# Performance work log

Hardware: AMD Instinct MI355X
Metric: run time of the kernel (lower is better)

## Reference

```python
import jax, jax.numpy as jnp
import numpy as np

N, C, H, W = 32, 256, 64, 64
STRIDE = 4  # slices of refs' H dim per block, as in the torch mem_save path
EPS = 1e-12  # F.normalize clamp_min eps


def setup_inputs() -> dict:
    key = jax.random.key(0)
    k1, k2 = jax.random.split(key)
    refs = jax.random.normal(k1, (N, C, H, W), dtype=jnp.float32)
    img = jax.random.normal(k2, (C, H, W), dtype=jnp.float32)
    return {"refs": refs, "img": img}


def _l2_normalize(x, axis):
    # matches torch.nn.functional.normalize(p=2): x / max(||x||, eps)
    n = jnp.sqrt(jnp.sum(x * x, axis=axis, keepdims=True))
    return x / jnp.maximum(n, EPS)


def reference(refs, img):
    # refs: (N, C, H, W), img: (C, H, W)
    refs_n = _l2_normalize(refs, axis=1)
    img_n = _l2_normalize(img, axis=0)

    img_flat = img_n.reshape(C, H * W).T  # (HW, C) query vectors

    # group reference feature vectors by blocks of STRIDE rows of refs' H dim:
    # (N,C,H,W) -> (H, N, W, C) -> (H//STRIDE, STRIDE*N*W, C)
    blocks = refs_n.transpose(2, 0, 3, 1).reshape(H // STRIDE, STRIDE * N * W, C)

    def step(running_max, block):
        # (HW, C) x (blocksize, C)^T -> (HW, blocksize) cosine sims
        sim = jnp.einsum('xc,yc->xy', img_flat, block)
        return jnp.maximum(running_max, sim.max(axis=1)), None

    init = jnp.full((H * W,), -jnp.inf, dtype=img_flat.dtype)
    best, _ = jax.lax.scan(step, init, blocks)
    return best.reshape(H, W)
```

## Files before the change

### kernel.cpp

```cpp
#include <hip/hip_runtime.h>

#define CN 256
#define HN 64
#define WN 64
#define NNW 32
#define HW (HN*WN)
#define NREF (NNW*HW)
#define KD 256

#define BMT 128
#define BNT 64
#define NCHV 16
#define NTILES (NREF/NCHV/BNT)

using bf16x8 = __attribute__((ext_vector_type(8))) short;
using f32x4  = __attribute__((ext_vector_type(4))) float;

__device__ inline unsigned short f2bf(float x) {
  unsigned int u = __float_as_uint(x);
  return (unsigned short)((u + 0x7fffu + ((u >> 16) & 1u)) >> 16);
}

__device__ inline void atomicMaxFloat(float* addr, float val) {
  if (val >= 0.f) atomicMax(reinterpret_cast<int*>(addr), __float_as_int(val));
  else            atomicMin(reinterpret_cast<unsigned int*>(addr), __float_as_uint(val));
}

__device__ inline void gload_lds16(const void* g, void* l) {
  __builtin_amdgcn_global_load_lds(
      (const __attribute__((address_space(1))) void*)g,
      (__attribute__((address_space(3))) void*)l, 16, 0, 0);
}

__global__ __launch_bounds__(256)
void norm_kernel(const float* __restrict__ refs, const float* __restrict__ img,
                 unsigned short* __restrict__ Rb, unsigned short* __restrict__ Qb,
                 float* __restrict__ out) {
  __shared__ float tile[CN][WN + 1];
  __shared__ float ssq[4][WN];
  __shared__ float scl[WN];
  const int bid = blockIdx.x;
  const int t = threadIdx.x;
  const float* src; unsigned short* dst; int nh;
  if (bid < NNW * HN) { src = refs; dst = Rb; nh = bid; }
  else {
    src = img; dst = Qb; nh = bid - NNW * HN;
    if (t < 64) out[(size_t)nh * 64 + t] = -INFINITY;
  }
  const float* base = src + (size_t)(nh >> 6) * (CN * (size_t)HW) + (size_t)(nh & 63) * WN;

  const int c16 = t >> 4, w4 = (t & 15) * 4;
#pragma unroll
  for (int j = 0; j < 16; ++j) {
    int c = j * 16 + c16;
    float4 v = *(const float4*)&base[(size_t)c * HW + w4];
    tile[c][w4 + 0] = v.x; tile[c][w4 + 1] = v.y;
    tile[c][w4 + 2] = v.z; tile[c][w4 + 3] = v.w;
  }
  __syncthreads();
  {
    int w = t & 63, vv = t >> 6;
    float s = 0.f;
#pragma unroll 8
    for (int cc = 0; cc < 64; ++cc) { float x = tile[vv * 64 + cc][w]; s += x * x; }
    ssq[vv][w] = s;
  }
  __syncthreads();
  if (t < 64)
    scl[t] = 1.f / fmaxf(sqrtf(ssq[0][t] + ssq[1][t] + ssq[2][t] + ssq[3][t]), 1e-12f);
  __syncthreads();
  const int w = t >> 2, cq = t & 3;
  unsigned short* orow = dst + ((size_t)nh * WN + w) * KD;
  const float sc = scl[w];
#pragma unroll
  for (int j = 0; j < 8; ++j) {
    int c0 = (j * 4 + cq) * 8;
    bf16x8 o;
#pragma unroll
    for (int k = 0; k < 8; ++k) o[k] = (short)f2bf(tile[c0 + k][w] * sc);
    *(bf16x8*)&orow[c0] = o;
  }
}

#define BARR() __builtin_amdgcn_s_barrier()
#define SCHED0() __builtin_amdgcn_sched_barrier(0)
#define GATE(N) asm volatile("s_waitcnt vmcnt(" #N ")" ::: "memory")
#define LGKM0() asm volatile("s_waitcnt lgkmcnt(0)" ::: "memory")

#define STGB(P, BT) do { \
  _Pragma("unroll") \
  for (int q = 0; q < 8; ++q) \
    gload_lds16(rsb + (BT) * 16384 + q * 2048, &lds[P][wid * 4096 + q * 512]); \
} while (0)

#define STRIP(P, NI) do { \
  bf16x8 bb[8]; \
  _Pragma("unroll") \
  for (int kf = 0; kf < 8; ++kf) \
    bb[kf] = *(const bf16x8*)&lds[P][(kf >> 1) * 4096 + ((NI) * 16 + l15) * 64 \
        + ((((kf & 1) * 4 + (lane >> 4)) ^ l7) * 8)]; \
  f32x4 acc0, acc1; \
  __builtin_amdgcn_s_setprio(1); \
  _Pragma("unroll") \
  for (int kf = 0; kf < 8; ++kf) { \
    acc0 = __builtin_amdgcn_mfma_f32_16x16x32_bf16(a[0][kf], bb[kf], kf ? acc0 : ZZ, 0, 0, 0); \
    acc1 = __builtin_amdgcn_mfma_f32_16x16x32_bf16(a[1][kf], bb[kf], kf ? acc1 : ZZ, 0, 0, 0); \
  } \
  __builtin_amdgcn_s_setprio(0); \
  _Pragma("unroll") \
  for (int ee = 0; ee < 4; ++ee) { \
    run0[ee] = fmaxf(run0[ee], acc0[ee]); \
    run1[ee] = fmaxf(run1[ee], acc1[ee]); \
  } \
} while (0)

#define STRIPS(P) do { STRIP(P, 0); STRIP(P, 1); STRIP(P, 2); STRIP(P, 3); } while (0)

__global__ __launch_bounds__(256, 2)
void simmax_kernel(const unsigned short* __restrict__ Q,
                   const unsigned short* __restrict__ R,
                   float* __restrict__ out) {
  __shared__ unsigned short lds[2][16384];

  const int t = threadIdx.x;
  const int lane = t & 63;
  const int wid = t >> 6;
  const int l15 = lane & 15;
  const int l7  = lane & 7;

  const int wg  = (blockIdx.x & 7) * 64 + (blockIdx.x >> 3);
  const int nch = wg >> 5;
  const int bm  = wg & 31;

  const int srow = lane >> 3;
  const int schunk = (lane & 7) ^ srow;
  const unsigned short* rsb = R + ((size_t)nch * 8192 + srow) * KD + wid * 64 + schunk * 8;

  const f32x4 ZZ = {0.f, 0.f, 0.f, 0.f};
  f32x4 run0, run1;
#pragma unroll
  for (int ee = 0; ee < 4; ++ee) { run0[ee] = -1e30f; run1[ee] = -1e30f; }

#pragma unroll
  for (int b = 0; b < 2; ++b) {
    const unsigned short* qsb = Q + (size_t)(bm * BMT + b * 64 + srow) * KD
                                  + wid * 64 + schunk * 8;
#pragma unroll
    for (int q = 0; q < 8; ++q)
      gload_lds16(qsb + q * 2048, &lds[b][wid * 4096 + q * 512]);
  }
  GATE(0); BARR(); SCHED0();

  bf16x8 a[2][8];
#pragma unroll
  for (int mi = 0; mi < 2; ++mi) {
    const int row = wid * 32 + mi * 16 + l15;
    const int r63 = row & 63;
#pragma unroll
    for (int kf = 0; kf < 8; ++kf)
      a[mi][kf] = *(const bf16x8*)&lds[wid >> 1][(kf >> 1) * 4096 + r63 * 64
          + ((((kf & 1) * 4 + (lane >> 4)) ^ l7) * 8)];
  }
  LGKM0(); BARR();

  STGB(0, 0);
  for (int bt = 0; bt < NTILES - 1; ++bt) {
    STGB((bt + 1) & 1, bt + 1);
    GATE(8); BARR(); SCHED0();
    STRIPS(bt & 1);
    BARR();
  }
  GATE(0); BARR(); SCHED0();
  STRIPS((NTILES - 1) & 1);

#pragma unroll
  for (int mi = 0; mi < 2; ++mi)
#pragma unroll
    for (int ee = 0; ee < 4; ++ee) {
      float v = mi ? run1[ee] : run0[ee];
      v = fmaxf(v, __shfl_xor(v, 1));
      v = fmaxf(v, __shfl_xor(v, 2));
      v = fmaxf(v, __shfl_xor(v, 4));
      v = fmaxf(v, __shfl_xor(v, 8));
      if (l15 == 0)
        atomicMaxFloat(&out[bm * BMT + wid * 32 + mi * 16 + (lane >> 4) * 4 + ee], v);
    }
}

extern "C" void kernel_launch(void* const* d_in, const int* in_sizes, int n_in,
                              void* d_out, int out_size, void* d_ws, size_t ws_size,
                              hipStream_t stream) {
  const float* refs = (const float*)d_in[0];
  const float* img  = (const float*)d_in[1];
  float* out = (float*)d_out;

  unsigned short* Rb = (unsigned short*)d_ws;
  unsigned short* Qb = Rb + (size_t)NREF * KD;

  hipLaunchKernelGGL(norm_kernel, dim3(NNW * HN + HN), dim3(256), 0, stream,
                     refs, img, Rb, Qb, out);
  hipLaunchKernelGGL(simmax_kernel, dim3(NCHV * (HW / BMT)), dim3(256), 0, stream,
                     Qb, Rb, out);
}
```

Baseline: 251.7 us.

## Double the query tile per workgroup to 256 rows and split refs into 32 chunks

Each workgroup now holds 256 query rows, 64 per wave as four 16-row MFMA fragments, instead of 128. Refs are split into 32 chunks so the grid size stays the same. Each staged reference tile is therefore reused across twice as many query rows, which halves total LDS and global traffic for the refs. In exchange, each wave keeps twice as many A-fragment registers (64 VGPRs for A), which raises register pressure and may limit occupancy.

Result: faster. 216.6 us (-14.0%).

```diff
diff --git a/kernel.cpp b/kernel.cpp
--- a/kernel.cpp
+++ b/kernel.cpp
@@ -8,9 +8,9 @@
 #define NREF (NNW*HW)
 #define KD 256
 
-#define BMT 128
+#define BMT 256
 #define BNT 64
-#define NCHV 16
+#define NCHV 32
 #define NTILES (NREF/NCHV/BNT)
 
 using bf16x8 = __attribute__((ext_vector_type(8))) short;
@@ -99,18 +99,22 @@
   for (int kf = 0; kf < 8; ++kf) \
     bb[kf] = *(const bf16x8*)&lds[P][(kf >> 1) * 4096 + ((NI) * 16 + l15) * 64 \
         + ((((kf & 1) * 4 + (lane >> 4)) ^ l7) * 8)]; \
-  f32x4 acc0, acc1; \
+  f32x4 ac0, ac1, ac2, ac3; \
   __builtin_amdgcn_s_setprio(1); \
   _Pragma("unroll") \
   for (int kf = 0; kf < 8; ++kf) { \
-    acc0 = __builtin_amdgcn_mfma_f32_16x16x32_bf16(a[0][kf], bb[kf], kf ? acc0 : ZZ, 0, 0, 0); \
-    acc1 = __builtin_amdgcn_mfma_f32_16x16x32_bf16(a[1][kf], bb[kf], kf ? acc1 : ZZ, 0, 0, 0); \
+    ac0 = __builtin_amdgcn_mfma_f32_16x16x32_bf16(a[0][kf], bb[kf], kf ? ac0 : ZZ, 0, 0, 0); \
+    ac1 = __builtin_amdgcn_mfma_f32_16x16x32_bf16(a[1][kf], bb[kf], kf ? ac1 : ZZ, 0, 0, 0); \
+    ac2 = __builtin_amdgcn_mfma_f32_16x16x32_bf16(a[2][kf], bb[kf], kf ? ac2 : ZZ, 0, 0, 0); \
+    ac3 = __builtin_amdgcn_mfma_f32_16x16x32_bf16(a[3][kf], bb[kf], kf ? ac3 : ZZ, 0, 0, 0); \
   } \
   __builtin_amdgcn_s_setprio(0); \
   _Pragma("unroll") \
   for (int ee = 0; ee < 4; ++ee) { \
-    run0[ee] = fmaxf(run0[ee], acc0[ee]); \
-    run1[ee] = fmaxf(run1[ee], acc1[ee]); \
+    run[0][ee] = fmaxf(run[0][ee], ac0[ee]); \
+    run[1][ee] = fmaxf(run[1][ee], ac1[ee]); \
+    run[2][ee] = fmaxf(run[2][ee], ac2[ee]); \
+    run[3][ee] = fmaxf(run[3][ee], ac3[ee]); \
   } \
 } while (0)
 
@@ -129,39 +133,43 @@
   const int l7  = lane & 7;
 
   const int wg  = (blockIdx.x & 7) * 64 + (blockIdx.x >> 3);
-  const int nch = wg >> 5;
-  const int bm  = wg & 31;
+  const int nch = wg >> 4;
+  const int bm  = wg & 15;
 
   const int srow = lane >> 3;
   const int schunk = (lane & 7) ^ srow;
-  const unsigned short* rsb = R + ((size_t)nch * 8192 + srow) * KD + wid * 64 + schunk * 8;
+  const unsigned short* rsb = R + ((size_t)nch * 4096 + srow) * KD + wid * 64 + schunk * 8;
 
   const f32x4 ZZ = {0.f, 0.f, 0.f, 0.f};
-  f32x4 run0, run1;
-#pragma unroll
-  for (int ee = 0; ee < 4; ++ee) { run0[ee] = -1e30f; run1[ee] = -1e30f; }
-
-#pragma unroll
-  for (int b = 0; b < 2; ++b) {
-    const unsigned short* qsb = Q + (size_t)(bm * BMT + b * 64 + srow) * KD
-                                  + wid * 64 + schunk * 8;
-#pragma unroll
-    for (int q = 0; q < 8; ++q)
-      gload_lds16(qsb + q * 2048, &lds[b][wid * 4096 + q * 512]);
-  }
-  GATE(0); BARR(); SCHED0();
-
-  bf16x8 a[2][8];
-#pragma unroll
-  for (int mi = 0; mi < 2; ++mi) {
-    const int row = wid * 32 + mi * 16 + l15;
-    const int r63 = row & 63;
-#pragma unroll
-    for (int kf = 0; kf < 8; ++kf)
-      a[mi][kf] = *(const bf16x8*)&lds[wid >> 1][(kf >> 1) * 4096 + r63 * 64
-          + ((((kf & 1) * 4 + (lane >> 4)) ^ l7) * 8)];
-  }
-  LGKM0(); BARR();
+  f32x4 run[4];
+#pragma unroll
+  for (int mi = 0; mi < 4; ++mi)
+#pragma unroll
+    for (int ee = 0; ee < 4; ++ee) run[mi][ee] = -1e30f;
+
+  bf16x8 a[4][8];
+#pragma unroll
+  for (int p = 0; p < 2; ++p) {
+#pragma unroll
+    for (int b = 0; b < 2; ++b) {
+      const unsigned short* qsb = Q + (size_t)(bm * BMT + p * 128 + b * 64 + srow) * KD
+                                    + wid * 64 + schunk * 8;
+#pragma unroll
+      for (int q = 0; q < 8; ++q)
+        gload_lds16(qsb + q * 2048, &lds[b][wid * 4096 + q * 512]);
+    }
+    GATE(0); BARR(); SCHED0();
+    if ((wid >> 1) == p) {
+      const int b = wid & 1;
+#pragma unroll
+      for (int mi = 0; mi < 4; ++mi)
+#pragma unroll
+        for (int kf = 0; kf < 8; ++kf)
+          a[mi][kf] = *(const bf16x8*)&lds[b][(kf >> 1) * 4096 + (mi * 16 + l15) * 64
+              + ((((kf & 1) * 4 + (lane >> 4)) ^ l7) * 8)];
+    }
+    LGKM0(); BARR();
+  }
 
   STGB(0, 0);
   for (int bt = 0; bt < NTILES - 1; ++bt) {
@@ -174,16 +182,16 @@
   STRIPS((NTILES - 1) & 1);
 
 #pragma unroll
-  for (int mi = 0; mi < 2; ++mi)
+  for (int mi = 0; mi < 4; ++mi)
 #pragma unroll
     for (int ee = 0; ee < 4; ++ee) {
-      float v = mi ? run1[ee] : run0[ee];
+      float v = run[mi][ee];
       v = fmaxf(v, __shfl_xor(v, 1));
       v = fmaxf(v, __shfl_xor(v, 2));
       v = fmaxf(v, __shfl_xor(v, 4));
       v = fmaxf(v, __shfl_xor(v, 8));
       if (l15 == 0)
-        atomicMaxFloat(&out[bm * BMT + wid * 32 + mi * 16 + (lane >> 4) * 4 + ee], v);
+        atomicMaxFloat(&out[bm * BMT + wid * 64 + mi * 16 + (lane >> 4) * 4 + ee], v);
     }
 }
 
```
